# Optimization experiments

Measured on AMD Instinct MI355X. Metric: run time of the kernel, lower is better.

## Reference

```python
import jax, jax.numpy as jnp
import numpy as np

KH, KW, PAD, DIL, STRIDE = 3, 3, 1, 1, 1


def _conv2d(x, w):
    # plain dense conv, NCHW / OIHW, stride 1, pad 1
    return jax.lax.conv_general_dilated(
        x, w, window_strides=(STRIDE, STRIDE),
        padding=[(PAD, PAD), (PAD, PAD)],
        rhs_dilation=(DIL, DIL),
        dimension_numbers=('NCHW', 'OIHW', 'NCHW'))


def _deform_patches(x, offset):
    """Bilinear-sample deformable patches.
    x: [B,C,H,W], offset: [B,2K,Ho,Wo] with per-tap (dy,dx).
    Returns [B,C,K,Ho,Wo]."""
    B, C, H, W = x.shape
    Ho, Wo = offset.shape[2], offset.shape[3]
    K = KH * KW
    off = offset.reshape(B, K, 2, Ho, Wo)

    ky = jnp.repeat(jnp.arange(KH), KW)            # [K]
    kx = jnp.tile(jnp.arange(KW), KH)              # [K]
    base_y = (jnp.arange(Ho) * STRIDE - PAD)[None, :, None] + (DIL * ky)[:, None, None]  # [K,Ho,1]
    base_x = (jnp.arange(Wo) * STRIDE - PAD)[None, None, :] + (DIL * kx)[:, None, None]  # [K,1,Wo]

    sy = base_y[None].astype(x.dtype) + off[:, :, 0]   # [B,K,Ho,Wo]
    sx = base_x[None].astype(x.dtype) + off[:, :, 1]

    y0 = jnp.floor(sy); x0 = jnp.floor(sx)
    ly = sy - y0;       lx = sx - x0
    y0i = y0.astype(jnp.int32); x0i = x0.astype(jnp.int32)

    x_flat = x.reshape(B, C, H * W)

    def corner(yi, xi, wgt):
        valid = (yi >= 0) & (yi < H) & (xi >= 0) & (xi < W)   # zero padding outside
        idx = (jnp.clip(yi, 0, H - 1) * W + jnp.clip(xi, 0, W - 1))  # [B,K,Ho,Wo]
        gath = jax.vmap(lambda img, i: img[:, i.reshape(-1)])(x_flat, idx)  # [B,C,K*Ho*Wo]
        gath = gath.reshape(B, C, K, Ho, Wo)
        return gath * (wgt * valid.astype(x.dtype))[:, None]

    p = corner(y0i,     x0i,     (1 - ly) * (1 - lx))
    p = p + corner(y0i,     x0i + 1, (1 - ly) * lx)
    p = p + corner(y0i + 1, x0i,     ly * (1 - lx))
    p = p + corner(y0i + 1, x0i + 1, ly * lx)
    return p  # [B,C,K,Ho,Wo]


def setup_inputs() -> dict:
    key = jax.random.key(0)
    k1, k2, k3 = jax.random.split(key, 3)
    B, C, H, W = 8, 256, 64, 64
    Cout = 256
    x = jax.random.normal(k1, (B, C, H, W), dtype=jnp.float32)
    offset_w = jax.random.normal(k2, (2 * KH * KW, C, KH, KW), dtype=jnp.float32) * 0.02
    deform_w = jax.random.normal(k3, (Cout, C, KH, KW), dtype=jnp.float32) * 0.02
    return {"x": x, "offset_w": offset_w, "deform_w": deform_w}


def reference(x, offset_w, deform_w):
    # 1) offset-predicting conv
    offset = _conv2d(x, offset_w)                    # [B,2K,H,W]
    # 2) deformable conv = bilinear gather + contraction over (Cin, K)
    patches = _deform_patches(x, offset)             # [B,C,K,H,W]
    Cout = deform_w.shape[0]
    wk = deform_w.reshape(Cout, deform_w.shape[1], KH * KW)
    y = jnp.einsum('bckhw,ock->bohw', patches, wk)   # [B,Cout,H,W]
    # 3) avg + std channel attention (torch.std default: unbiased, ddof=1)
    avg = jnp.mean(y, axis=(2, 3), keepdims=True)
    std = jnp.std(y, axis=(2, 3), keepdims=True, ddof=1)
    attn = jax.nn.sigmoid(avg + std)
    return y * attn
```

## Files before the change

kernel.cpp:

```cpp
#include <hip/hip_runtime.h>
#include <hip/hip_bf16.h>
#include <math.h>

#define C_IN 256
#define H_   64
#define W_   64
#define B_   8
#define COUT 256
#define HW   (H_*W_)

typedef float f32x4 __attribute__((ext_vector_type(4)));
typedef short short8 __attribute__((ext_vector_type(8)));

static __device__ __forceinline__ int pack_bf16x2(float a, float b) {
    __hip_bfloat162 h = __float22bfloat162_rn(make_float2(a, b));
    union { __hip_bfloat162 h; int i; } u; u.h = h;
    return u.i;
}

static __device__ __forceinline__ void unpk(int v, float& lo, float& hi) {
    union { int i; float f; } a, b;
    a.i = v << 16;
    b.i = v & 0xffff0000;
    lo = a.f; hi = b.f;
}

__global__ __launch_bounds__(256) void prep_weights_kernel(
    const float* __restrict__ ow, const float* __restrict__ dw,
    short* __restrict__ wR, short* __restrict__ wO)
{
    int blk = blockIdx.x;
    int k   = blk / 288;
    int row = blk % 288;
    int c   = threadIdx.x;
    union { float f; unsigned u; } a;
    if (row < 256) {
        a.f = dw[(size_t)row * 2304 + c * 9 + k];
        unsigned r = (a.u + 0x7fffu + ((a.u >> 16) & 1u)) >> 16;
        wR[(size_t)k * 65536 + row * 256 + c] = (short)r;
    } else {
        int o = row - 256;
        a.f = (o < 18) ? ow[(size_t)o * 2304 + c * 9 + k] : 0.f;
        unsigned r = (a.u + 0x7fffu + ((a.u >> 16) & 1u)) >> 16;
        wO[(size_t)k * 8192 + o * 256 + c] = (short)r;
    }
}

__global__ __launch_bounds__(256) void transpose_x_kernel(
    const float* __restrict__ x, unsigned short* __restrict__ xT)
{
    __shared__ float tile[64][257];
    const int tid = threadIdx.x;
    const int b = blockIdx.x >> 6, h = blockIdx.x & 63;
    const float* xb = x + ((size_t)b << 20) + h * 64;

#pragma unroll
    for (int pass = 0; pass < 16; ++pass) {
        int c  = pass * 16 + (tid >> 4);
        int w0 = (tid & 15) * 4;
        float4 v = *(const float4*)(xb + (size_t)c * 4096 + w0);
        tile[w0][c] = v.x; tile[w0 + 1][c] = v.y;
        tile[w0 + 2][c] = v.z; tile[w0 + 3][c] = v.w;
    }
    __syncthreads();

    int4* ob = (int4*)(xT + ((size_t)blockIdx.x << 14));
#pragma unroll
    for (int pass = 0; pass < 8; ++pass) {
        int idx = pass * 256 + tid;
        int w = idx >> 5, ch8 = idx & 31;
        const float* tr = &tile[w][ch8 * 8];
        int4 pk;
        pk.x = pack_bf16x2(tr[0], tr[1]);
        pk.y = pack_bf16x2(tr[2], tr[3]);
        pk.z = pack_bf16x2(tr[4], tr[5]);
        pk.w = pack_bf16x2(tr[6], tr[7]);
        ob[idx] = pk;
    }
}

__global__ __launch_bounds__(256, 2) void offset_mfma_kernel(
    const unsigned short* __restrict__ xT, const short* __restrict__ wO,
    float* __restrict__ offs)
{
    __shared__ int4 aT[32 * 8];
    __shared__ int4 bT[64 * 8];

    const int tid = threadIdx.x;
    const int b   = blockIdx.x & 7;
    const int ho  = blockIdx.x >> 3;

    const int px = tid >> 2;
    const int cg = tid & 3;
    const int wv = tid >> 6;
    const int ln = tid & 63;
    const int lo = ln & 15;
    const int quad = ln >> 4;

    f32x4 acc[2];
    acc[0] = (f32x4){0.f, 0.f, 0.f, 0.f};
    acc[1] = (f32x4){0.f, 0.f, 0.f, 0.f};

    const unsigned short* xbb = xT + ((size_t)b << 20);
    const int oA = tid >> 3, octA = tid & 7;
    const int4 zero4 = {0, 0, 0, 0};

    for (int s = 0; s < 36; ++s) {
        int k  = s >> 2;
        int c0 = (s & 3) << 6;
        int yy = ho + k / 3 - 1;
        int xx = px + k % 3 - 1;
        bool valid = (yy >= 0) & (yy < 64) & (xx >= 0) & (xx < 64);
        int yc = min(max(yy, 0), 63), xc = min(max(xx, 0), 63);

        const int4* src = (const int4*)(xbb + (((size_t)yc * 64 + xc) << 8) + c0 + cg * 16);
        int4 p0 = valid ? src[0] : zero4;
        int4 p1 = valid ? src[1] : zero4;
        bT[px * 8 + ((2 * cg)     ^ (px & 7))] = p0;
        bT[px * 8 + ((2 * cg + 1) ^ (px & 7))] = p1;

        aT[oA * 8 + (octA ^ (oA & 7))] =
            *(const int4*)(wO + (size_t)k * 8192 + oA * 256 + c0 + octA * 8);
        __syncthreads();

        int pxl = wv * 16 + lo;
#pragma unroll
        for (int ks = 0; ks < 2; ++ks) {
            int ch = ks * 4 + quad;
            short8 bfr = *(const short8*)&bT[pxl * 8 + (ch ^ (pxl & 7))];
#pragma unroll
            for (int t = 0; t < 2; ++t) {
                int o = t * 16 + lo;
                short8 afr = *(const short8*)&aT[o * 8 + (ch ^ (o & 7))];
                acc[t] = __builtin_amdgcn_mfma_f32_16x16x32_bf16(afr, bfr, acc[t], 0, 0, 0);
            }
        }
        __syncthreads();
    }

#pragma unroll
    for (int t = 0; t < 2; ++t) {
#pragma unroll
        for (int r = 0; r < 4; ++r) {
            int o = t * 16 + quad * 4 + r;
            if (o < 18)
                offs[((size_t)b * 18 + o) * HW + ho * 64 + wv * 16 + lo] = acc[t][r];
        }
    }
}

__global__ __launch_bounds__(256, 2) void deform_mfma_kernel(
    const unsigned short* __restrict__ xT, const float* __restrict__ offs,
    const short* __restrict__ wR, float* __restrict__ y,
    float* __restrict__ sum_, float* __restrict__ sumsq_)
{
    __shared__ int4   meta_i[576];
    __shared__ float4 meta_w[576];
    __shared__ int4   aT[256 * 8];
    __shared__ int4   bT[64 * 8];

    const int tid = threadIdx.x;
    const int b   = blockIdx.x & 7;
    const int ho  = blockIdx.x >> 3;

    for (int e = tid; e < 576; e += 256) {
        int kk = e >> 6;
        int pxe = e & 63;
        float dy = offs[((size_t)b * 18 + 2 * kk)     * HW + ho * W_ + pxe];
        float dx = offs[((size_t)b * 18 + 2 * kk + 1) * HW + ho * W_ + pxe];
        float sy = (float)(ho - 1 + kk / 3) + dy;
        float sx = (float)(pxe - 1 + kk % 3) + dx;
        float y0f = floorf(sy), x0f = floorf(sx);
        float ly = sy - y0f, lx = sx - x0f;
        int y0 = (int)y0f, x0 = (int)x0f;
        int y1 = y0 + 1, x1 = x0 + 1;
        float wy0 = 1.f - ly, wy1 = ly, wx0 = 1.f - lx, wx1 = lx;
        bool vy0 = (y0 >= 0) & (y0 < H_), vy1 = (y1 >= 0) & (y1 < H_);
        bool vx0 = (x0 >= 0) & (x0 < W_), vx1 = (x1 >= 0) & (x1 < W_);
        int cy0 = min(max(y0, 0), H_ - 1), cy1 = min(max(y1, 0), H_ - 1);
        int cx0 = min(max(x0, 0), W_ - 1), cx1 = min(max(x1, 0), W_ - 1);
        int4 ii; float4 ww;
        ii.x = cy0 * W_ + cx0;  ww.x = wy0 * wx0 * ((vy0 & vx0) ? 1.f : 0.f);
        ii.y = cy0 * W_ + cx1;  ww.y = wy0 * wx1 * ((vy0 & vx1) ? 1.f : 0.f);
        ii.z = cy1 * W_ + cx0;  ww.z = wy1 * wx0 * ((vy1 & vx0) ? 1.f : 0.f);
        ii.w = cy1 * W_ + cx1;  ww.w = wy1 * wx1 * ((vy1 & vx1) ? 1.f : 0.f);
        meta_i[e] = ii;
        meta_w[e] = ww;
    }

    const int px = tid >> 2;
    const int cg = tid & 3;
    const int wv = tid >> 6;
    const int ln = tid & 63;
    const int lo = ln & 15;
    const int quad = ln >> 4;

    f32x4 acc[4][4];
#pragma unroll
    for (int t = 0; t < 4; ++t)
#pragma unroll
        for (int p = 0; p < 4; ++p)
            acc[t][p] = (f32x4){0.f, 0.f, 0.f, 0.f};

    const unsigned short* xbb = xT + ((size_t)b << 20) + cg * 16;
    const int oA = tid >> 3, octA = tid & 7;

    __syncthreads();

    for (int s = 0; s < 36; ++s) {
        int k  = s >> 2;
        int c0 = (s & 3) << 6;

        int4   ii = meta_i[k * 64 + px];
        float4 ww = meta_w[k * 64 + px];

        const unsigned short* xc0 = xbb + c0;
        const int4* pA = (const int4*)(xc0 + ((size_t)ii.x << 8));
        const int4* pB = (const int4*)(xc0 + ((size_t)ii.y << 8));
        const int4* pC = (const int4*)(xc0 + ((size_t)ii.z << 8));
        const int4* pD = (const int4*)(xc0 + ((size_t)ii.w << 8));
        int4 a0 = pA[0], a1 = pA[1];
        int4 b0 = pB[0], b1 = pB[1];
        int4 cc0 = pC[0], cc1 = pC[1];
        int4 d0 = pD[0], d1 = pD[1];

        auto blend = [&](int av, int bv, int cv, int dv) -> int {
            float alo, ahi, blo, bhi, clo, chi, dlo, dhi;
            unpk(av, alo, ahi); unpk(bv, blo, bhi);
            unpk(cv, clo, chi); unpk(dv, dlo, dhi);
            float vlo = ww.x * alo + ww.y * blo + ww.z * clo + ww.w * dlo;
            float vhi = ww.x * ahi + ww.y * bhi + ww.z * chi + ww.w * dhi;
            return pack_bf16x2(vlo, vhi);
        };
        int4 o0, o1;
        o0.x = blend(a0.x, b0.x, cc0.x, d0.x);
        o0.y = blend(a0.y, b0.y, cc0.y, d0.y);
        o0.z = blend(a0.z, b0.z, cc0.z, d0.z);
        o0.w = blend(a0.w, b0.w, cc0.w, d0.w);
        o1.x = blend(a1.x, b1.x, cc1.x, d1.x);
        o1.y = blend(a1.y, b1.y, cc1.y, d1.y);
        o1.z = blend(a1.z, b1.z, cc1.z, d1.z);
        o1.w = blend(a1.w, b1.w, cc1.w, d1.w);
        bT[px * 8 + ((2 * cg)     ^ (px & 7))] = o0;
        bT[px * 8 + ((2 * cg + 1) ^ (px & 7))] = o1;

        const short* wk = wR + (size_t)k * 65536 + c0;
#pragma unroll
        for (int it = 0; it < 8; ++it) {
            int o = oA + it * 32;
            aT[o * 8 + (octA ^ (o & 7))] = *(const int4*)(wk + o * 256 + octA * 8);
        }
        __syncthreads();

#pragma unroll
        for (int ks = 0; ks < 2; ++ks) {
            int ch = ks * 4 + quad;
            short8 afr[4], bfr[4];
#pragma unroll
            for (int t = 0; t < 4; ++t) {
                int o = wv * 64 + t * 16 + lo;
                afr[t] = *(const short8*)&aT[o * 8 + (ch ^ (o & 7))];
                int p = t * 16 + lo;
                bfr[t] = *(const short8*)&bT[p * 8 + (ch ^ (p & 7))];
            }
#pragma unroll
            for (int t = 0; t < 4; ++t)
#pragma unroll
                for (int p = 0; p < 4; ++p)
                    acc[t][p] = __builtin_amdgcn_mfma_f32_16x16x32_bf16(
                        afr[t], bfr[p], acc[t][p], 0, 0, 0);
        }
        __syncthreads();
    }

    float* yb = y + ((size_t)b << 20) + ho * 64;
#pragma unroll
    for (int t = 0; t < 4; ++t) {
#pragma unroll
        for (int r = 0; r < 4; ++r) {
            int o = wv * 64 + t * 16 + quad * 4 + r;
            float sv = 0.f, qv = 0.f;
#pragma unroll
            for (int p = 0; p < 4; ++p) {
                float val = acc[t][p][r];
                yb[(size_t)o * HW + p * 16 + lo] = val;
                sv += val;
                qv += val * val;
            }
#pragma unroll
            for (int m = 1; m <= 8; m <<= 1) {
                sv += __shfl_xor(sv, m, 16);
                qv += __shfl_xor(qv, m, 16);
            }
            if (lo == 0) {
                atomicAdd(&sum_[b * COUT + o], sv);
                atomicAdd(&sumsq_[b * COUT + o], qv);
            }
        }
    }
}

__global__ __launch_bounds__(256) void attn_scale_kernel(
    const float* __restrict__ sum_, const float* __restrict__ sumsq_,
    float* __restrict__ y)
{
    int bo = blockIdx.x;
    float s = sum_[bo], q = sumsq_[bo];
    float mean = s * (1.f / 4096.f);
    float var  = (q - s * s * (1.f / 4096.f)) * (1.f / 4095.f);
    float sd   = sqrtf(fmaxf(var, 0.f));
    float attn = 1.f / (1.f + expf(-(mean + sd)));
    float4* yp = (float4*)(y + (size_t)bo * HW);
#pragma unroll
    for (int i = 0; i < 4; ++i) {
        float4 v = yp[threadIdx.x + i * 256];
        v.x *= attn; v.y *= attn; v.z *= attn; v.w *= attn;
        yp[threadIdx.x + i * 256] = v;
    }
}

extern "C" void kernel_launch(void* const* d_in, const int* in_sizes, int n_in,
                              void* d_out, int out_size, void* d_ws, size_t ws_size,
                              hipStream_t stream)
{
    const float* x  = (const float*)d_in[0];
    const float* ow = (const float*)d_in[1];
    const float* dw = (const float*)d_in[2];
    float* out = (float*)d_out;
    float* ws  = (float*)d_ws;

    float*          offs = ws;
    unsigned short* xT   = (unsigned short*)(ws + 589824);
    short*          wR   = (short*)(xT + 8388608);
    short*          wO   = wR + 589824;
    float*          sum_ = (float*)(wO + 73728);
    float*          sumsq_ = sum_ + 2048;

    hipMemsetAsync(sum_, 0, 2 * 2048 * sizeof(float), stream);

    prep_weights_kernel<<<9 * 288, 256, 0, stream>>>(ow, dw, wR, wO);
    transpose_x_kernel<<<512, 256, 0, stream>>>(x, xT);
    offset_mfma_kernel<<<512, 256, 0, stream>>>(xT, wO, offs);
    deform_mfma_kernel<<<512, 256, 0, stream>>>(xT, offs, wR, out, sum_, sumsq_);
    attn_scale_kernel<<<2048, 256, 0, stream>>>(sum_, sumsq_, out);
}
```

Before: 197.1 us.

## Pre-swizzle weights into MFMA fragment order, double-buffer B, halve deform tile

Weights are rewritten at prep time into a layout that matches the MFMA A-fragment, so both MFMA kernels load A operands directly from global memory and no longer stage them in LDS. The sampled B tile is double-buffered: the next step's gather is issued before the current step's MFMAs and blended afterwards, which leaves one barrier per step. The deform kernel now handles 32 pixels per block with 1024 blocks and a higher occupancy hint. Costs are more redundant global and L2 weight traffic per block and a smaller per-block tile, which lowers weight reuse.

```diff
diff --git a/kernel.cpp b/kernel.cpp
--- a/kernel.cpp
+++ b/kernel.cpp
@@ -33,16 +33,22 @@
     int k   = blk / 288;
     int row = blk % 288;
     int c   = threadIdx.x;
+    int cblk = c >> 6, ks = (c >> 5) & 1, q = (c >> 3) & 3, ce = c & 7;
     union { float f; unsigned u; } a;
     if (row < 256) {
-        a.f = dw[(size_t)row * 2304 + c * 9 + k];
+        int o = row;
+        a.f = dw[(size_t)o * 2304 + c * 9 + k];
         unsigned r = (a.u + 0x7fffu + ((a.u >> 16) & 1u)) >> 16;
-        wR[(size_t)k * 65536 + row * 256 + c] = (short)r;
+        size_t idx = (size_t)(k * 8 + cblk * 2 + ks) * 8192
+                   + (size_t)(o >> 4) * 512 + q * 128 + (o & 15) * 8 + ce;
+        wR[idx] = (short)r;
     } else {
         int o = row - 256;
         a.f = (o < 18) ? ow[(size_t)o * 2304 + c * 9 + k] : 0.f;
         unsigned r = (a.u + 0x7fffu + ((a.u >> 16) & 1u)) >> 16;
-        wO[(size_t)k * 8192 + o * 256 + c] = (short)r;
+        size_t idx = (size_t)(k * 8 + cblk * 2 + ks) * 1024
+                   + (size_t)(o >> 4) * 512 + q * 128 + (o & 15) * 8 + ce;
+        wO[idx] = (short)r;
     }
 }
 
@@ -83,8 +89,7 @@
     const unsigned short* __restrict__ xT, const short* __restrict__ wO,
     float* __restrict__ offs)
 {
-    __shared__ int4 aT[32 * 8];
-    __shared__ int4 bT[64 * 8];
+    __shared__ int4 bT[2][64 * 8];
 
     const int tid = threadIdx.x;
     const int b   = blockIdx.x & 7;
@@ -96,42 +101,44 @@
     const int ln = tid & 63;
     const int lo = ln & 15;
     const int quad = ln >> 4;
+    const int pxl = wv * 16 + lo;
 
     f32x4 acc[2];
     acc[0] = (f32x4){0.f, 0.f, 0.f, 0.f};
     acc[1] = (f32x4){0.f, 0.f, 0.f, 0.f};
 
     const unsigned short* xbb = xT + ((size_t)b << 20);
-    const int oA = tid >> 3, octA = tid & 7;
     const int4 zero4 = {0, 0, 0, 0};
 
-    for (int s = 0; s < 36; ++s) {
-        int k  = s >> 2;
-        int c0 = (s & 3) << 6;
+    auto stageB = [&](int s, int buf) {
+        int k = s >> 2, c0 = (s & 3) << 6;
         int yy = ho + k / 3 - 1;
         int xx = px + k % 3 - 1;
         bool valid = (yy >= 0) & (yy < 64) & (xx >= 0) & (xx < 64);
         int yc = min(max(yy, 0), 63), xc = min(max(xx, 0), 63);
-
         const int4* src = (const int4*)(xbb + (((size_t)yc * 64 + xc) << 8) + c0 + cg * 16);
         int4 p0 = valid ? src[0] : zero4;
         int4 p1 = valid ? src[1] : zero4;
-        bT[px * 8 + ((2 * cg)     ^ (px & 7))] = p0;
-        bT[px * 8 + ((2 * cg + 1) ^ (px & 7))] = p1;
-
-        aT[oA * 8 + (octA ^ (oA & 7))] =
-            *(const int4*)(wO + (size_t)k * 8192 + oA * 256 + c0 + octA * 8);
-        __syncthreads();
-
-        int pxl = wv * 16 + lo;
+        bT[buf][px * 8 + ((2 * cg)     ^ (px & 7))] = p0;
+        bT[buf][px * 8 + ((2 * cg + 1) ^ (px & 7))] = p1;
+    };
+
+    stageB(0, 0);
+    __syncthreads();
+
+    for (int s = 0; s < 36; ++s) {
+        const int cur = s & 1;
+        if (s < 35) stageB(s + 1, cur ^ 1);
+
+        const int k = s >> 2;
+        const short* wkb = wO + (size_t)(k * 8 + (s & 3) * 2) * 1024 + ln * 8;
 #pragma unroll
         for (int ks = 0; ks < 2; ++ks) {
             int ch = ks * 4 + quad;
-            short8 bfr = *(const short8*)&bT[pxl * 8 + (ch ^ (pxl & 7))];
+            short8 bfr = *(const short8*)&bT[cur][pxl * 8 + (ch ^ (pxl & 7))];
 #pragma unroll
             for (int t = 0; t < 2; ++t) {
-                int o = t * 16 + lo;
-                short8 afr = *(const short8*)&aT[o * 8 + (ch ^ (o & 7))];
+                short8 afr = *(const short8*)(wkb + ks * 1024 + t * 512);
                 acc[t] = __builtin_amdgcn_mfma_f32_16x16x32_bf16(afr, bfr, acc[t], 0, 0, 0);
             }
         }
@@ -149,23 +156,24 @@
     }
 }
 
-__global__ __launch_bounds__(256, 2) void deform_mfma_kernel(
+__global__ __launch_bounds__(256, 4) void deform_mfma_kernel(
     const unsigned short* __restrict__ xT, const float* __restrict__ offs,
     const short* __restrict__ wR, float* __restrict__ y,
     float* __restrict__ sum_, float* __restrict__ sumsq_)
 {
-    __shared__ int4   meta_i[576];
-    __shared__ float4 meta_w[576];
-    __shared__ int4   aT[256 * 8];
-    __shared__ int4   bT[64 * 8];
+    __shared__ int4   meta_i[288];
+    __shared__ float4 meta_w[288];
+    __shared__ int4   bT[2][32 * 8];
 
     const int tid = threadIdx.x;
     const int b   = blockIdx.x & 7;
-    const int ho  = blockIdx.x >> 3;
-
-    for (int e = tid; e < 576; e += 256) {
-        int kk = e >> 6;
-        int pxe = e & 63;
+    const int ho  = (blockIdx.x >> 3) & 63;
+    const int xh  = blockIdx.x >> 9;
+    const int px0 = xh * 32;
+
+    for (int e = tid; e < 288; e += 256) {
+        int kk  = e >> 5;
+        int pxe = px0 + (e & 31);
         float dy = offs[((size_t)b * 18 + 2 * kk)     * HW + ho * W_ + pxe];
         float dx = offs[((size_t)b * 18 + 2 * kk + 1) * HW + ho * W_ + pxe];
         float sy = (float)(ho - 1 + kk / 3) + dy;
@@ -174,106 +182,115 @@
         float ly = sy - y0f, lx = sx - x0f;
         int y0 = (int)y0f, x0 = (int)x0f;
         int y1 = y0 + 1, x1 = x0 + 1;
-        float wy0 = 1.f - ly, wy1 = ly, wx0 = 1.f - lx, wx1 = lx;
+        float wy0 = 1.f - ly, wx0 = 1.f - lx;
         bool vy0 = (y0 >= 0) & (y0 < H_), vy1 = (y1 >= 0) & (y1 < H_);
         bool vx0 = (x0 >= 0) & (x0 < W_), vx1 = (x1 >= 0) & (x1 < W_);
         int cy0 = min(max(y0, 0), H_ - 1), cy1 = min(max(y1, 0), H_ - 1);
         int cx0 = min(max(x0, 0), W_ - 1), cx1 = min(max(x1, 0), W_ - 1);
         int4 ii; float4 ww;
         ii.x = cy0 * W_ + cx0;  ww.x = wy0 * wx0 * ((vy0 & vx0) ? 1.f : 0.f);
-        ii.y = cy0 * W_ + cx1;  ww.y = wy0 * wx1 * ((vy0 & vx1) ? 1.f : 0.f);
-        ii.z = cy1 * W_ + cx0;  ww.z = wy1 * wx0 * ((vy1 & vx0) ? 1.f : 0.f);
-        ii.w = cy1 * W_ + cx1;  ww.w = wy1 * wx1 * ((vy1 & vx1) ? 1.f : 0.f);
+        ii.y = cy0 * W_ + cx1;  ww.y = wy0 * lx  * ((vy0 & vx1) ? 1.f : 0.f);
+        ii.z = cy1 * W_ + cx0;  ww.z = ly  * wx0 * ((vy1 & vx0) ? 1.f : 0.f);
+        ii.w = cy1 * W_ + cx1;  ww.w = ly  * lx  * ((vy1 & vx1) ? 1.f : 0.f);
         meta_i[e] = ii;
         meta_w[e] = ww;
     }
 
-    const int px = tid >> 2;
-    const int cg = tid & 3;
+    const int px = tid >> 3;
+    const int cg = tid & 7;
     const int wv = tid >> 6;
     const int ln = tid & 63;
     const int lo = ln & 15;
     const int quad = ln >> 4;
 
-    f32x4 acc[4][4];
+    f32x4 acc[4][2];
 #pragma unroll
     for (int t = 0; t < 4; ++t)
 #pragma unroll
-        for (int p = 0; p < 4; ++p)
+        for (int p = 0; p < 2; ++p)
             acc[t][p] = (f32x4){0.f, 0.f, 0.f, 0.f};
 
-    const unsigned short* xbb = xT + ((size_t)b << 20) + cg * 16;
-    const int oA = tid >> 3, octA = tid & 7;
+    const unsigned short* xbb = xT + ((size_t)b << 20) + cg * 8;
+
+    int4 gA, gB, gC, gD;
+    float4 ww;
+    auto blend = [&](int av, int bv, int cv, int dv) -> int {
+        float alo, ahi, blo, bhi, clo, chi, dlo, dhi;
+        unpk(av, alo, ahi); unpk(bv, blo, bhi);
+        unpk(cv, clo, chi); unpk(dv, dlo, dhi);
+        float vlo = ww.x * alo + ww.y * blo + ww.z * clo + ww.w * dlo;
+        float vhi = ww.x * ahi + ww.y * bhi + ww.z * chi + ww.w * dhi;
+        return pack_bf16x2(vlo, vhi);
+    };
 
     __syncthreads();
 
+    {
+        int4 ii = meta_i[px];
+        ww = meta_w[px];
+        gA = *(const int4*)(xbb + ((size_t)ii.x << 8));
+        gB = *(const int4*)(xbb + ((size_t)ii.y << 8));
+        gC = *(const int4*)(xbb + ((size_t)ii.z << 8));
+        gD = *(const int4*)(xbb + ((size_t)ii.w << 8));
+        int4 o0;
+        o0.x = blend(gA.x, gB.x, gC.x, gD.x);
+        o0.y = blend(gA.y, gB.y, gC.y, gD.y);
+        o0.z = blend(gA.z, gB.z, gC.z, gD.z);
+        o0.w = blend(gA.w, gB.w, gC.w, gD.w);
+        bT[0][px * 8 + (cg ^ (px & 7))] = o0;
+    }
+    __syncthreads();
+
     for (int s = 0; s < 36; ++s) {
-        int k  = s >> 2;
-        int c0 = (s & 3) << 6;
-
-        int4   ii = meta_i[k * 64 + px];
-        float4 ww = meta_w[k * 64 + px];
-
-        const unsigned short* xc0 = xbb + c0;
-        const int4* pA = (const int4*)(xc0 + ((size_t)ii.x << 8));
-        const int4* pB = (const int4*)(xc0 + ((size_t)ii.y << 8));
-        const int4* pC = (const int4*)(xc0 + ((size_t)ii.z << 8));
-        const int4* pD = (const int4*)(xc0 + ((size_t)ii.w << 8));
-        int4 a0 = pA[0], a1 = pA[1];
-        int4 b0 = pB[0], b1 = pB[1];
-        int4 cc0 = pC[0], cc1 = pC[1];
-        int4 d0 = pD[0], d1 = pD[1];
-
-        auto blend = [&](int av, int bv, int cv, int dv) -> int {
-            float alo, ahi, blo, bhi, clo, chi, dlo, dhi;
-            unpk(av, alo, ahi); unpk(bv, blo, bhi);
-            unpk(cv, clo, chi); unpk(dv, dlo, dhi);
-            float vlo = ww.x * alo + ww.y * blo + ww.z * clo + ww.w * dlo;
-            float vhi = ww.x * ahi + ww.y * bhi + ww.z * chi + ww.w * dhi;
-            return pack_bf16x2(vlo, vhi);
-        };
-        int4 o0, o1;
-        o0.x = blend(a0.x, b0.x, cc0.x, d0.x);
-        o0.y = blend(a0.y, b0.y, cc0.y, d0.y);
-        o0.z = blend(a0.z, b0.z, cc0.z, d0.z);
-        o0.w = blend(a0.w, b0.w, cc0.w, d0.w);
-        o1.x = blend(a1.x, b1.x, cc1.x, d1.x);
-        o1.y = blend(a1.y, b1.y, cc1.y, d1.y);
-        o1.z = blend(a1.z, b1.z, cc1.z, d1.z);
-        o1.w = blend(a1.w, b1.w, cc1.w, d1.w);
-        bT[px * 8 + ((2 * cg)     ^ (px & 7))] = o0;
-        bT[px * 8 + ((2 * cg + 1) ^ (px & 7))] = o1;
-
-        const short* wk = wR + (size_t)k * 65536 + c0;
-#pragma unroll
-        for (int it = 0; it < 8; ++it) {
-            int o = oA + it * 32;
-            aT[o * 8 + (octA ^ (o & 7))] = *(const int4*)(wk + o * 256 + octA * 8);
-        }
-        __syncthreads();
-
+        const int cur = s & 1;
+        const bool hasNext = (s < 35);
+
+        if (hasNext) {
+            int sn = s + 1;
+            int kn = sn >> 2, cn = (sn & 3) << 6;
+            int4 ii = meta_i[kn * 32 + px];
+            ww = meta_w[kn * 32 + px];
+            const unsigned short* xc = xbb + cn;
+            gA = *(const int4*)(xc + ((size_t)ii.x << 8));
+            gB = *(const int4*)(xc + ((size_t)ii.y << 8));
+            gC = *(const int4*)(xc + ((size_t)ii.z << 8));
+            gD = *(const int4*)(xc + ((size_t)ii.w << 8));
+        }
+
+        const int k = s >> 2;
+        const short* wkb = wR + (size_t)(k * 8 + (s & 3) * 2) * 8192
+                         + wv * 2048 + ln * 8;
 #pragma unroll
         for (int ks = 0; ks < 2; ++ks) {
             int ch = ks * 4 + quad;
-            short8 afr[4], bfr[4];
+            short8 bfr[2];
+#pragma unroll
+            for (int p = 0; p < 2; ++p) {
+                int pp = p * 16 + lo;
+                bfr[p] = *(const short8*)&bT[cur][pp * 8 + (ch ^ (pp & 7))];
+            }
 #pragma unroll
             for (int t = 0; t < 4; ++t) {
-                int o = wv * 64 + t * 16 + lo;
-                afr[t] = *(const short8*)&aT[o * 8 + (ch ^ (o & 7))];
-                int p = t * 16 + lo;
-                bfr[t] = *(const short8*)&bT[p * 8 + (ch ^ (p & 7))];
-            }
-#pragma unroll
-            for (int t = 0; t < 4; ++t)
-#pragma unroll
-                for (int p = 0; p < 4; ++p)
+                short8 afr = *(const short8*)(wkb + ks * 8192 + t * 512);
+#pragma unroll
+                for (int p = 0; p < 2; ++p)
                     acc[t][p] = __builtin_amdgcn_mfma_f32_16x16x32_bf16(
-                        afr[t], bfr[p], acc[t][p], 0, 0, 0);
+                        afr, bfr[p], acc[t][p], 0, 0, 0);
+            }
+        }
+
+        if (hasNext) {
+            int4 o0;
+            o0.x = blend(gA.x, gB.x, gC.x, gD.x);
+            o0.y = blend(gA.y, gB.y, gC.y, gD.y);
+            o0.z = blend(gA.z, gB.z, gC.z, gD.z);
+            o0.w = blend(gA.w, gB.w, gC.w, gD.w);
+            bT[cur ^ 1][px * 8 + (cg ^ (px & 7))] = o0;
         }
         __syncthreads();
     }
 
-    float* yb = y + ((size_t)b << 20) + ho * 64;
+    float* yb = y + ((size_t)b << 20) + ho * 64 + px0;
 #pragma unroll
     for (int t = 0; t < 4; ++t) {
 #pragma unroll
@@ -281,7 +298,7 @@
             int o = wv * 64 + t * 16 + quad * 4 + r;
             float sv = 0.f, qv = 0.f;
 #pragma unroll
-            for (int p = 0; p < 4; ++p) {
+            for (int p = 0; p < 2; ++p) {
                 float val = acc[t][p][r];
                 yb[(size_t)o * HW + p * 16 + lo] = val;
                 sv += val;
@@ -341,6 +358,6 @@
     prep_weights_kernel<<<9 * 288, 256, 0, stream>>>(ow, dw, wR, wO);
     transpose_x_kernel<<<512, 256, 0, stream>>>(x, xT);
     offset_mfma_kernel<<<512, 256, 0, stream>>>(xT, wO, offs);
-    deform_mfma_kernel<<<512, 256, 0, stream>>>(xT, offs, wR, out, sum_, sumsq_);
+    deform_mfma_kernel<<<1024, 256, 0, stream>>>(xT, offs, wR, out, sum_, sumsq_);
     attn_scale_kernel<<<2048, 256, 0, stream>>>(sum_, sumsq_, out);
 }
```

New measurement: 200.6 us. Within noise of the previous version (+1.7%).
